# Kernel tuning notes

Hardware: AMD Instinct MI355X
Metric: run time of the kernel (lower is better)

Reference implementation:

```python
import jax, jax.numpy as jnp
import numpy as np

B, S, D = 4, 2048, 1024
H = 16
HD = D // H  # 64


def setup_inputs() -> dict:
    key = jax.random.key(0)
    ks = jax.random.split(key, 4)
    scale = 0.02
    return {
        "hidden_states": jax.random.normal(ks[0], (B, S, D), dtype=jnp.float32),
        "attention_mask": jnp.zeros((B, 1, 1, S), dtype=jnp.float32),
        "Wq": jax.random.normal(ks[1], (D, D), dtype=jnp.float32) * scale,
        "bq": jnp.zeros((D,), dtype=jnp.float32),
        "Wk": jax.random.normal(ks[2], (D, D), dtype=jnp.float32) * scale,
        "bk": jnp.zeros((D,), dtype=jnp.float32),
        "Wv": jax.random.normal(ks[3], (D, D), dtype=jnp.float32) * scale,
        "bv": jnp.zeros((D,), dtype=jnp.float32),
    }


def reference(hidden_states, attention_mask, Wq, bq, Wk, bk, Wv, bv):
    # linear projections: x @ W^T + b (torch nn.Linear convention); here W stored as [D,D]
    def proj(x, W, b):
        y = jnp.einsum("bsd,ed->bse", x, W) + b
        # [B,S,D] -> [B,H,S,HD]
        return y.reshape(B, S, H, HD).transpose(0, 2, 1, 3)

    q = proj(hidden_states, Wq, bq)
    k = proj(hidden_states, Wk, bk)
    v = proj(hidden_states, Wv, bv)

    scores = jnp.einsum("bhqd,bhkd->bhqk", q, k) / jnp.sqrt(jnp.float32(HD))
    scores = scores + attention_mask  # additive mask broadcast [B,1,1,S]
    probs = jax.nn.softmax(scores, axis=-1)  # dropout p=0 -> identity
    ctx = jnp.einsum("bhqk,bhkd->bhqd", probs, v)
    ctx = ctx.transpose(0, 2, 1, 3).reshape(B, S, D)
    return ctx
```

## Files before the change

### kernel.cpp

```cpp
#include <hip/hip_runtime.h>
#include <hip/hip_bf16.h>

typedef __attribute__((ext_vector_type(4))) float f32x4;
typedef __attribute__((ext_vector_type(8))) short bf16x8;
typedef __attribute__((ext_vector_type(8))) unsigned short u16x8;
typedef unsigned short u16;

#define DEV static __device__ __forceinline__

DEV u16 f2bf(float f) {
    union { float f; unsigned int u; } v; v.f = f;
    unsigned int r = v.u + 0x7FFFu + ((v.u >> 16) & 1u);
    return (u16)(r >> 16);
}

DEV unsigned int cvt_pk(float lo, float hi) {
    unsigned int r;
    asm("v_cvt_pk_bf16_f32 %0, %1, %2" : "=v"(r) : "v"(lo), "v"(hi));
    return r;
}

DEV void async16(const void* g, void* l) {
    __builtin_amdgcn_global_load_lds((const __attribute__((address_space(1))) unsigned int*)g,
                                     (__attribute__((address_space(3))) unsigned int*)l, 16, 0, 0);
}

__global__ void cvt_all(const float4* __restrict__ x, const float4* __restrict__ wq,
                        const float4* __restrict__ wk, const float4* __restrict__ wv,
                        ushort4* __restrict__ xb, ushort4* __restrict__ wb,
                        const float* __restrict__ mask, float* __restrict__ em) {
    int bid = blockIdx.x;
    if (bid >= 11264) {
        int i = (bid - 11264) * 256 + threadIdx.x;
        em[i] = __builtin_amdgcn_exp2f(mask[i] * 1.44269504088896340736f);
        return;
    }
    const float4* s;
    ushort4* d;
    int i;
    if (bid < 8192) {
        s = x; d = xb; i = bid * 256 + threadIdx.x;
    } else {
        int r = bid - 8192;
        int wsel = r >> 10;
        s = (wsel == 0) ? wq : (wsel == 1) ? wk : wv;
        d = wb + (size_t)wsel * 262144;
        i = (r & 1023) * 256 + threadIdx.x;
    }
    float4 v = s[i];
    ushort4 o;
    o.x = f2bf(v.x); o.y = f2bf(v.y); o.z = f2bf(v.z); o.w = f2bf(v.w);
    d[i] = o;
}

__launch_bounds__(256, 2)
__global__ void qkv_gemm(const u16* __restrict__ xb, const u16* __restrict__ wb,
                         const float* __restrict__ bq, const float* __restrict__ bk,
                         const float* __restrict__ bv, const float* __restrict__ em,
                         u16* __restrict__ Qb, u16* __restrict__ Kb, u16* __restrict__ Vtb) {
    __shared__ u16 Al[2][128 * 64];
    __shared__ u16 Bl[2][128 * 64];
    const int t = threadIdx.x, ln = t & 63, w = t >> 6;
    const int wr = w >> 1, wc = w & 1;
    const int m0 = blockIdx.x * 128, e0 = blockIdx.y * 128, p = blockIdx.z;
    const u16* Wp = wb + (size_t)p * 1048576;
    const float* bias = (p == 0) ? bq : (p == 1) ? bk : bv;

    const int srow = t >> 3, scol = (t & 7) * 8;

    f32x4 acc[4][4];
#pragma unroll
    for (int i = 0; i < 4; i++)
#pragma unroll
        for (int j = 0; j < 4; j++) acc[i][j] = (f32x4){0.f, 0.f, 0.f, 0.f};

#define G_STAGE(buf, kk)                                                              \
    {                                                                                 \
        _Pragma("unroll")                                                             \
        for (int c = 0; c < 4; c++) {                                                 \
            int r = c * 32 + srow;                                                    \
            async16(&xb[(size_t)(m0 + r) * 1024 + (kk) + scol], &Al[buf][r * 64 + scol]); \
            async16(&Wp[(size_t)(e0 + r) * 1024 + (kk) + scol], &Bl[buf][r * 64 + scol]); \
        }                                                                             \
    }

    G_STAGE(0, 0);
    __syncthreads();
    int cur = 0;
    for (int kt = 0; kt < 16; kt++) {
        if (kt < 15) G_STAGE(cur ^ 1, (kt + 1) * 64);
#pragma unroll
        for (int kc = 0; kc < 2; kc++) {
            bf16x8 a[4], bb[4];
#pragma unroll
            for (int mf = 0; mf < 4; mf++)
                a[mf] = *(const bf16x8*)&Al[cur][(wr * 64 + mf * 16 + (ln & 15)) * 64 + kc * 32 + (ln >> 4) * 8];
#pragma unroll
            for (int nf = 0; nf < 4; nf++)
                bb[nf] = *(const bf16x8*)&Bl[cur][(wc * 64 + nf * 16 + (ln & 15)) * 64 + kc * 32 + (ln >> 4) * 8];
            __builtin_amdgcn_s_setprio(1);
#pragma unroll
            for (int mf = 0; mf < 4; mf++)
#pragma unroll
                for (int nf = 0; nf < 4; nf++)
                    acc[mf][nf] = __builtin_amdgcn_mfma_f32_16x16x32_bf16(a[mf], bb[nf], acc[mf][nf], 0, 0, 0);
            __builtin_amdgcn_s_setprio(0);
        }
        __syncthreads();
        cur ^= 1;
    }
#undef G_STAGE

    const int q16 = ln & 15, g = ln >> 4;
    if (p == 2) {
#pragma unroll
        for (int nf = 0; nf < 4; nf++) {
            int e = e0 + wc * 64 + nf * 16 + q16;
            float bias_v = bias[e];
            int h = e >> 6, hd = e & 63;
#pragma unroll
            for (int mf = 0; mf < 4; mf++) {
                int m = m0 + wr * 64 + mf * 16 + g * 4;
                int b = m >> 11, s = m & 2047;
                f32x4 emv = *(const f32x4*)&em[b * 2048 + s];
                ushort4 pk;
                pk.x = f2bf((acc[mf][nf][0] + bias_v) * emv[0]);
                pk.y = f2bf((acc[mf][nf][1] + bias_v) * emv[1]);
                pk.z = f2bf((acc[mf][nf][2] + bias_v) * emv[2]);
                pk.w = f2bf((acc[mf][nf][3] + bias_v) * emv[3]);
                *(ushort4*)&Vtb[((size_t)((b * 16 + h) * 64 + hd)) * 2048 + s] = pk;
            }
        }
    } else {
        const float qscale = (p == 0) ? 0.18033688011112042f : 1.0f;
        u16* out = (p == 0) ? Qb : Kb;
#pragma unroll
        for (int nf = 0; nf < 4; nf++) {
            int e = e0 + wc * 64 + nf * 16 + q16;
            float bias_v = bias[e];
            int h = e >> 6, hd = e & 63;
#pragma unroll
            for (int mf = 0; mf < 4; mf++) {
#pragma unroll
                for (int r = 0; r < 4; r++) {
                    int m = m0 + wr * 64 + mf * 16 + g * 4 + r;
                    int b = m >> 11, s = m & 2047;
                    out[((size_t)(b * 16 + h) * 2048 + s) * 64 + hd] = f2bf((acc[mf][nf][r] + bias_v) * qscale);
                }
            }
        }
    }
}

__launch_bounds__(128, 2)
__global__ void attn_kernel(const u16* __restrict__ Q, const u16* __restrict__ K,
                            const u16* __restrict__ Vt, const float* __restrict__ em,
                            float* __restrict__ out) {
    __shared__ u16 Kl[2][64 * 64];
    __shared__ u16 Vl[2][64 * 64];
    __shared__ u16 Pl[2][32 * 64];
    const int t = threadIdx.x, ln = t & 63, w = t >> 6;
    const int q16 = ln & 15, g = ln >> 4;

    const int bid0 = blockIdx.x;
    const int swz = (bid0 & 7) * 128 + (bid0 >> 3);
    const int qbi = swz & 15, bh = swz >> 4;
    const int b = bh >> 4, h = bh & 15;
    const int qr = qbi * 128 + w * 64;
    const size_t base = (size_t)bh * 2048 * 64;

    bf16x8 aq[4][2];
#pragma unroll
    for (int mf = 0; mf < 4; mf++)
#pragma unroll
        for (int dc = 0; dc < 2; dc++)
            aq[mf][dc] = *(const bf16x8*)&Q[base + (size_t)(qr + mf * 16 + q16) * 64 + dc * 32 + g * 8];

    const int rbase = t >> 3;
    const int sc = (t & 7) ^ (rbase & 7);

    const int swz0 = (g ^ (q16 & 7)) * 8;
    const int swz1 = ((g ^ 4) ^ (q16 & 7)) * 8;

#define A_STAGE(buf, kk)                                                                   \
    {                                                                                      \
        _Pragma("unroll")                                                                  \
        for (int i = 0; i < 4; i++) {                                                      \
            int row = i * 16 + rbase;                                                      \
            async16(&K[base + (size_t)((kk) + row) * 64 + sc * 8], &Kl[buf][(i * 128 + t) * 8]); \
            async16(&Vt[base + (size_t)row * 2048 + (kk) + sc * 8], &Vl[buf][(i * 128 + t) * 8]); \
        }                                                                                  \
    }

    f32x4 accT[4][4];
    f32x4 lacc[4];
#pragma unroll
    for (int nf = 0; nf < 4; nf++)
#pragma unroll
        for (int mf = 0; mf < 4; mf++) accT[nf][mf] = (f32x4){0.f, 0.f, 0.f, 0.f};
#pragma unroll
    for (int mf = 0; mf < 4; mf++) lacc[mf] = (f32x4){0.f, 0.f, 0.f, 0.f};

    A_STAGE(0, 0);
    __syncthreads();
    int cur = 0;

    for (int kt = 0; kt < 32; kt++) {
        const int k0 = kt * 64;
        if (kt < 31) A_STAGE(cur ^ 1, k0 + 64);

        f32x4 em4[4];
#pragma unroll
        for (int kf = 0; kf < 4; kf++)
            em4[kf] = *(const f32x4*)&em[b * 2048 + k0 + kf * 16 + g * 4];

        bf16x8 ka[4][2];
#pragma unroll
        for (int kf = 0; kf < 4; kf++) {
            ka[kf][0] = *(const bf16x8*)&Kl[cur][(kf * 16 + q16) * 64 + swz0];
            ka[kf][1] = *(const bf16x8*)&Kl[cur][(kf * 16 + q16) * 64 + swz1];
        }

#pragma unroll
        for (int half = 0; half < 2; half++) {
#pragma unroll
            for (int mf2 = 0; mf2 < 2; mf2++) {
                const int mf = half * 2 + mf2;
                f32x4 st[4];
                __builtin_amdgcn_s_setprio(1);
#pragma unroll
                for (int kf = 0; kf < 4; kf++) {
                    f32x4 z = (f32x4){0.f, 0.f, 0.f, 0.f};
                    z = __builtin_amdgcn_mfma_f32_16x16x32_bf16(ka[kf][0], aq[mf][0], z, 0, 0, 0);
                    z = __builtin_amdgcn_mfma_f32_16x16x32_bf16(ka[kf][1], aq[mf][1], z, 0, 0, 0);
                    st[kf] = z;
                }
                __builtin_amdgcn_s_setprio(0);
#pragma unroll
                for (int kf = 0; kf < 4; kf++)
#pragma unroll
                    for (int r = 0; r < 4; r++)
                        st[kf][r] = __builtin_amdgcn_exp2f(st[kf][r]);
#pragma unroll
                for (int kf = 0; kf < 4; kf++)
                    lacc[mf] += st[kf] * em4[kf];
#pragma unroll
                for (int kf = 0; kf < 4; kf++) {
                    uint2 pk;
                    pk.x = cvt_pk(st[kf][0], st[kf][1]);
                    pk.y = cvt_pk(st[kf][2], st[kf][3]);
                    *(uint2*)&Pl[w][(mf2 * 16 + q16) * 64 + ((kf * 16 + g * 4) ^ ((q16 & 7) << 3))] = pk;
                }
            }

            __builtin_amdgcn_s_setprio(1);
#pragma unroll
            for (int kc = 0; kc < 2; kc++) {
                const int so = kc ? swz1 : swz0;
                bf16x8 bv4[4], pa[2];
#pragma unroll
                for (int nf = 0; nf < 4; nf++)
                    bv4[nf] = *(const bf16x8*)&Vl[cur][(nf * 16 + q16) * 64 + so];
#pragma unroll
                for (int mf2 = 0; mf2 < 2; mf2++)
                    pa[mf2] = *(const bf16x8*)&Pl[w][(mf2 * 16 + q16) * 64 + so];
#pragma unroll
                for (int nf = 0; nf < 4; nf++)
#pragma unroll
                    for (int mf2 = 0; mf2 < 2; mf2++)
                        accT[nf][half * 2 + mf2] =
                            __builtin_amdgcn_mfma_f32_16x16x32_bf16(bv4[nf], pa[mf2], accT[nf][half * 2 + mf2], 0, 0, 0);
            }
            __builtin_amdgcn_s_setprio(0);
        }

        __syncthreads();
        cur ^= 1;
    }
#undef A_STAGE

#pragma unroll
    for (int mf = 0; mf < 4; mf++) {
        float l = (lacc[mf][0] + lacc[mf][1]) + (lacc[mf][2] + lacc[mf][3]);
        l += __shfl_xor(l, 16);
        l += __shfl_xor(l, 32);
        float inv = 1.0f / l;
        int q = qr + mf * 16 + q16;
#pragma unroll
        for (int nf = 0; nf < 4; nf++) {
            f32x4 o = accT[nf][mf] * inv;
            *(f32x4*)&out[((size_t)(b * 2048 + q)) * 1024 + h * 64 + nf * 16 + g * 4] = o;
        }
    }
}

extern "C" void kernel_launch(void* const* d_in, const int* in_sizes, int n_in,
                              void* d_out, int out_size, void* d_ws, size_t ws_size,
                              hipStream_t stream) {
    const float* x    = (const float*)d_in[0];
    const float* mask = (const float*)d_in[1];
    const float* Wq   = (const float*)d_in[2];
    const float* bq   = (const float*)d_in[3];
    const float* Wk   = (const float*)d_in[4];
    const float* bk   = (const float*)d_in[5];
    const float* Wv   = (const float*)d_in[6];
    const float* bv   = (const float*)d_in[7];
    float* out = (float*)d_out;

    char* ws = (char*)d_ws;
    if (ws_size < (size_t)73433088) return;
    u16* xb   = (u16*)(ws);
    u16* wb   = (u16*)(ws + 16777216);
    u16* Qb   = (u16*)(ws + 23068672);
    u16* Kb   = (u16*)(ws + 39845888);
    u16* Vtb  = (u16*)(ws + 56623104);
    float* em = (float*)(ws + 73400320);

    cvt_all<<<11296, 256, 0, stream>>>((const float4*)x, (const float4*)Wq, (const float4*)Wk,
                                       (const float4*)Wv, (ushort4*)xb, (ushort4*)wb, mask, em);
    qkv_gemm<<<dim3(64, 8, 3), 256, 0, stream>>>(xb, wb, bq, bk, bv, em, Qb, Kb, Vtb);
    attn_kernel<<<1024, 128, 0, stream>>>(Qb, Kb, Vtb, em, out);
}
```

Baseline: 170.2 us.

## Switch attention to 32x32x16 MFMA and keep P in registers via permlane swap

```diff
diff --git a/kernel.cpp b/kernel.cpp
--- a/kernel.cpp
+++ b/kernel.cpp
@@ -2,8 +2,9 @@
 #include <hip/hip_bf16.h>
 
 typedef __attribute__((ext_vector_type(4))) float f32x4;
+typedef __attribute__((ext_vector_type(16))) float f32x16;
 typedef __attribute__((ext_vector_type(8))) short bf16x8;
-typedef __attribute__((ext_vector_type(8))) unsigned short u16x8;
+typedef __attribute__((ext_vector_type(4))) unsigned int u32x4;
 typedef unsigned short u16;
 
 #define DEV static __device__ __forceinline__
@@ -18,6 +19,10 @@
     unsigned int r;
     asm("v_cvt_pk_bf16_f32 %0, %1, %2" : "=v"(r) : "v"(lo), "v"(hi));
     return r;
+}
+
+DEV void pswap(unsigned int& a, unsigned int& b) {
+    asm volatile("v_permlane32_swap_b32 %0, %1" : "+v"(a), "+v"(b));
 }
 
 DEV void async16(const void* g, void* l) {
@@ -158,9 +163,8 @@
                             float* __restrict__ out) {
     __shared__ u16 Kl[2][64 * 64];
     __shared__ u16 Vl[2][64 * 64];
-    __shared__ u16 Pl[2][32 * 64];
     const int t = threadIdx.x, ln = t & 63, w = t >> 6;
-    const int q16 = ln & 15, g = ln >> 4;
+    const int ln31 = ln & 31, hi = ln >> 5, ln7 = ln & 7;
 
     const int bid0 = blockIdx.x;
     const int swz = (bid0 & 7) * 128 + (bid0 >> 3);
@@ -169,18 +173,15 @@
     const int qr = qbi * 128 + w * 64;
     const size_t base = (size_t)bh * 2048 * 64;
 
-    bf16x8 aq[4][2];
-#pragma unroll
-    for (int mf = 0; mf < 4; mf++)
-#pragma unroll
-        for (int dc = 0; dc < 2; dc++)
-            aq[mf][dc] = *(const bf16x8*)&Q[base + (size_t)(qr + mf * 16 + q16) * 64 + dc * 32 + g * 8];
+    bf16x8 aq[2][4];
+#pragma unroll
+    for (int qt = 0; qt < 2; qt++)
+#pragma unroll
+        for (int ds = 0; ds < 4; ds++)
+            aq[qt][ds] = *(const bf16x8*)&Q[base + (size_t)(qr + qt * 32 + ln31) * 64 + ds * 16 + hi * 8];
 
     const int rbase = t >> 3;
     const int sc = (t & 7) ^ (rbase & 7);
-
-    const int swz0 = (g ^ (q16 & 7)) * 8;
-    const int swz1 = ((g ^ 4) ^ (q16 & 7)) * 8;
 
 #define A_STAGE(buf, kk)                                                                   \
     {                                                                                      \
@@ -192,14 +193,14 @@
         }                                                                                  \
     }
 
-    f32x4 accT[4][4];
-    f32x4 lacc[4];
-#pragma unroll
-    for (int nf = 0; nf < 4; nf++)
-#pragma unroll
-        for (int mf = 0; mf < 4; mf++) accT[nf][mf] = (f32x4){0.f, 0.f, 0.f, 0.f};
-#pragma unroll
-    for (int mf = 0; mf < 4; mf++) lacc[mf] = (f32x4){0.f, 0.f, 0.f, 0.f};
+    f32x16 accT[2][2];
+    f32x4 lacc[2];
+#pragma unroll
+    for (int dt = 0; dt < 2; dt++)
+#pragma unroll
+        for (int qt = 0; qt < 2; qt++) accT[dt][qt] = (f32x16){};
+    lacc[0] = (f32x4){0.f, 0.f, 0.f, 0.f};
+    lacc[1] = (f32x4){0.f, 0.f, 0.f, 0.f};
 
     A_STAGE(0, 0);
     __syncthreads();
@@ -209,67 +210,63 @@
         const int k0 = kt * 64;
         if (kt < 31) A_STAGE(cur ^ 1, k0 + 64);
 
-        f32x4 em4[4];
-#pragma unroll
-        for (int kf = 0; kf < 4; kf++)
-            em4[kf] = *(const f32x4*)&em[b * 2048 + k0 + kf * 16 + g * 4];
-
-        bf16x8 ka[4][2];
-#pragma unroll
-        for (int kf = 0; kf < 4; kf++) {
-            ka[kf][0] = *(const bf16x8*)&Kl[cur][(kf * 16 + q16) * 64 + swz0];
-            ka[kf][1] = *(const bf16x8*)&Kl[cur][(kf * 16 + q16) * 64 + swz1];
-        }
-
-#pragma unroll
-        for (int half = 0; half < 2; half++) {
-#pragma unroll
-            for (int mf2 = 0; mf2 < 2; mf2++) {
-                const int mf = half * 2 + mf2;
-                f32x4 st[4];
+#pragma unroll
+        for (int kti = 0; kti < 2; kti++) {
+            bf16x8 ka[4];
+#pragma unroll
+            for (int ds = 0; ds < 4; ds++)
+                ka[ds] = *(const bf16x8*)&Kl[cur][(kti * 32 + ln31) * 64 + (((ds << 1) | hi) ^ ln7) * 8];
+
+            f32x4 em4[4];
+#pragma unroll
+            for (int rf = 0; rf < 4; rf++)
+                em4[rf] = *(const f32x4*)&em[b * 2048 + k0 + kti * 32 + rf * 8 + hi * 4];
+
+            u32x4 pb[2][2];
+#pragma unroll
+            for (int qt = 0; qt < 2; qt++) {
+                f32x16 z = (f32x16){};
                 __builtin_amdgcn_s_setprio(1);
 #pragma unroll
-                for (int kf = 0; kf < 4; kf++) {
-                    f32x4 z = (f32x4){0.f, 0.f, 0.f, 0.f};
-                    z = __builtin_amdgcn_mfma_f32_16x16x32_bf16(ka[kf][0], aq[mf][0], z, 0, 0, 0);
-                    z = __builtin_amdgcn_mfma_f32_16x16x32_bf16(ka[kf][1], aq[mf][1], z, 0, 0, 0);
-                    st[kf] = z;
+                for (int ds = 0; ds < 4; ds++)
+                    z = __builtin_amdgcn_mfma_f32_32x32x16_bf16(ka[ds], aq[qt][ds], z, 0, 0, 0);
+                __builtin_amdgcn_s_setprio(0);
+
+                float p[16];
+#pragma unroll
+                for (int i = 0; i < 16; i++) p[i] = __builtin_amdgcn_exp2f(z[i]);
+
+#pragma unroll
+                for (int rf = 0; rf < 4; rf++) {
+                    lacc[qt][0] += p[4 * rf + 0] * em4[rf][0];
+                    lacc[qt][1] += p[4 * rf + 1] * em4[rf][1];
+                    lacc[qt][2] += p[4 * rf + 2] * em4[rf][2];
+                    lacc[qt][3] += p[4 * rf + 3] * em4[rf][3];
                 }
-                __builtin_amdgcn_s_setprio(0);
-#pragma unroll
-                for (int kf = 0; kf < 4; kf++)
-#pragma unroll
-                    for (int r = 0; r < 4; r++)
-                        st[kf][r] = __builtin_amdgcn_exp2f(st[kf][r]);
-#pragma unroll
-                for (int kf = 0; kf < 4; kf++)
-                    lacc[mf] += st[kf] * em4[kf];
-#pragma unroll
-                for (int kf = 0; kf < 4; kf++) {
-                    uint2 pk;
-                    pk.x = cvt_pk(st[kf][0], st[kf][1]);
-                    pk.y = cvt_pk(st[kf][2], st[kf][3]);
-                    *(uint2*)&Pl[w][(mf2 * 16 + q16) * 64 + ((kf * 16 + g * 4) ^ ((q16 & 7) << 3))] = pk;
+
+                unsigned int pk00 = cvt_pk(p[0], p[1]),  pk01 = cvt_pk(p[2], p[3]);
+                unsigned int pk10 = cvt_pk(p[4], p[5]),  pk11 = cvt_pk(p[6], p[7]);
+                unsigned int pk20 = cvt_pk(p[8], p[9]),  pk21 = cvt_pk(p[10], p[11]);
+                unsigned int pk30 = cvt_pk(p[12], p[13]), pk31 = cvt_pk(p[14], p[15]);
+                pswap(pk00, pk10); pswap(pk01, pk11);
+                pswap(pk20, pk30); pswap(pk21, pk31);
+                pb[qt][0][0] = pk00; pb[qt][0][1] = pk01; pb[qt][0][2] = pk10; pb[qt][0][3] = pk11;
+                pb[qt][1][0] = pk20; pb[qt][1][1] = pk21; pb[qt][1][2] = pk30; pb[qt][1][3] = pk31;
+            }
+
+            __builtin_amdgcn_s_setprio(1);
+#pragma unroll
+            for (int s = 0; s < 2; s++) {
+#pragma unroll
+                for (int dt = 0; dt < 2; dt++) {
+                    bf16x8 va = *(const bf16x8*)&Vl[cur][(dt * 32 + ln31) * 64 +
+                                                         ((kti * 4 + s * 2 + hi) ^ ln7) * 8];
+#pragma unroll
+                    for (int qt = 0; qt < 2; qt++) {
+                        bf16x8 pv = *(const bf16x8*)&pb[qt][s];
+                        accT[dt][qt] = __builtin_amdgcn_mfma_f32_32x32x16_bf16(va, pv, accT[dt][qt], 0, 0, 0);
+                    }
                 }
-            }
-
-            __builtin_amdgcn_s_setprio(1);
-#pragma unroll
-            for (int kc = 0; kc < 2; kc++) {
-                const int so = kc ? swz1 : swz0;
-                bf16x8 bv4[4], pa[2];
-#pragma unroll
-                for (int nf = 0; nf < 4; nf++)
-                    bv4[nf] = *(const bf16x8*)&Vl[cur][(nf * 16 + q16) * 64 + so];
-#pragma unroll
-                for (int mf2 = 0; mf2 < 2; mf2++)
-                    pa[mf2] = *(const bf16x8*)&Pl[w][(mf2 * 16 + q16) * 64 + so];
-#pragma unroll
-                for (int nf = 0; nf < 4; nf++)
-#pragma unroll
-                    for (int mf2 = 0; mf2 < 2; mf2++)
-                        accT[nf][half * 2 + mf2] =
-                            __builtin_amdgcn_mfma_f32_16x16x32_bf16(bv4[nf], pa[mf2], accT[nf][half * 2 + mf2], 0, 0, 0);
             }
             __builtin_amdgcn_s_setprio(0);
         }
@@ -280,16 +277,22 @@
 #undef A_STAGE
 
 #pragma unroll
-    for (int mf = 0; mf < 4; mf++) {
-        float l = (lacc[mf][0] + lacc[mf][1]) + (lacc[mf][2] + lacc[mf][3]);
-        l += __shfl_xor(l, 16);
+    for (int qt = 0; qt < 2; qt++) {
+        float l = (lacc[qt][0] + lacc[qt][1]) + (lacc[qt][2] + lacc[qt][3]);
         l += __shfl_xor(l, 32);
         float inv = 1.0f / l;
-        int q = qr + mf * 16 + q16;
-#pragma unroll
-        for (int nf = 0; nf < 4; nf++) {
-            f32x4 o = accT[nf][mf] * inv;
-            *(f32x4*)&out[((size_t)(b * 2048 + q)) * 1024 + h * 64 + nf * 16 + g * 4] = o;
+        int q = qr + qt * 32 + ln31;
+#pragma unroll
+        for (int dt = 0; dt < 2; dt++) {
+#pragma unroll
+            for (int rf = 0; rf < 4; rf++) {
+                f32x4 o;
+                o[0] = accT[dt][qt][4 * rf + 0] * inv;
+                o[1] = accT[dt][qt][4 * rf + 1] * inv;
+                o[2] = accT[dt][qt][4 * rf + 2] * inv;
+                o[3] = accT[dt][qt][4 * rf + 3] * inv;
+                *(f32x4*)&out[((size_t)(b * 2048 + q)) * 1024 + h * 64 + dt * 32 + rf * 8 + hi * 4] = o;
+            }
         }
     }
 }
```

Result: no change. 172.7 us (+1.5%).
